# Kernel tuning notes

Hardware: AMD Instinct MI355X
Metric: run time of the kernel (lower is better)

The kernel has to match this reference:

```python
import jax, jax.numpy as jnp
import numpy as np

C = 64
SHIFT = 3
NEIGHBOR_SIZES = (3, 5, 7)  # dilation = 1 for all levels
NUM_GROUPS = 8


def conv2d(x, w, b, padding=0, groups=1):
    out = jax.lax.conv_general_dilated(
        x, w, (1, 1), [(padding, padding), (padding, padding)],
        dimension_numbers=('NCHW', 'OIHW', 'NCHW'),
        feature_group_count=groups)
    return out + b[None, :, None, None]


def natten_level(q, k, v, rpb, ks):
    # q,k,v: (B,H,W,C) channels-last; rpb: (2ks-1, 2ks-1); dilation=1.
    # NATTEN semantics: window of size ks x ks centered at each query, clamped
    # (shifted) at image borders so it always lies fully inside the image.
    B, H, W, Cc = q.shape
    r = ks // 2
    i = jnp.arange(H); ni = jnp.clip(i - r, 0, H - ks)   # window row starts
    j = jnp.arange(W); nj = jnp.clip(j - r, 0, W - ks)   # window col starts
    ar = jnp.arange(ks)
    ii = ni[:, None] + ar[None, :]                        # (H,ks) neighbor rows
    jj = nj[:, None] + ar[None, :]                        # (W,ks) neighbor cols
    kn = k[:, ii][:, :, :, jj]                            # (B,H,ks,W,ks,C)
    attn = jnp.einsum('bhwc,bhpwqc->bhwpq', q, kn)        # (B,H,W,ks,ks)
    # relative-position-bias lookup: row start pi = (ks-1) + ni - i
    pi = (ks - 1) + ni - i                                # (H,)
    pj = (ks - 1) + nj - j                                # (W,)
    bias = rpb[(pi[:, None] + ar[None, :])[:, None, :, None],
               (pj[:, None] + ar[None, :])[None, :, None, :]]  # (H,W,ks,ks)
    attn = attn + bias[None]
    attn = jax.nn.softmax(attn.reshape(B, H, W, ks * ks), axis=-1)
    attn = attn.reshape(B, H, W, ks, ks)
    vn = v[:, ii][:, :, :, jj]                            # (B,H,ks,W,ks,C)
    return jnp.einsum('bhwpq,bhpwqc->bhwc', attn, vn)


def _forward(sup_frame, key_frame, conv_smooth_w, conv_smooth_b,
             conv_reduce_w, conv_reduce_b, v_w0, v_b0, v_w1, v_b1,
             v_w2, v_b2, rpb0, rpb1, rpb2, fusion_w, fusion_b):
    p = SHIFT
    outs = [sup_frame]  # original (pre-shift) support features
    # shift-roll spatial correlation
    shifts = [(sh, sw) for sh in (-p, 0, p) for sw in (-p, 0, p)
              if not (sh == 0 and sw == 0)]
    padded = jnp.pad(sup_frame, ((0, 0), (0, 0), (p, p), (p, p)))
    parts = jnp.split(padded, NUM_GROUPS, axis=1)
    shifted = jnp.concatenate(
        [jnp.roll(parts[g], shifts[g], axis=(2, 3)) for g in range(NUM_GROUPS)],
        axis=1)[..., p:-p, p:-p]
    shifted = conv2d(shifted, conv_smooth_w, conv_smooth_b, padding=1,
                     groups=NUM_GROUPS)
    sup2 = conv2d(jnp.concatenate([sup_frame, shifted], axis=1),
                  conv_reduce_w, conv_reduce_b)
    # multi-scale neighborhood attention (single head)
    q = jnp.transpose(key_frame, (0, 2, 3, 1))
    k = jnp.transpose(sup2, (0, 2, 3, 1))
    v_ws = (v_w0, v_w1, v_w2); v_bs = (v_b0, v_b1, v_b2)
    rpbs = (rpb0, rpb1, rpb2)
    for lvl, ks in enumerate(NEIGHBOR_SIZES):
        v = jnp.transpose(conv2d(sup2, v_ws[lvl], v_bs[lvl]), (0, 2, 3, 1))
        agg = natten_level(q, k, v, rpbs[lvl], ks)
        outs.append(jnp.transpose(agg, (0, 3, 1, 2)))
    fused = jnp.concatenate(outs, axis=1)  # (B, 4*C, H, W)
    return jax.nn.relu(conv2d(fused, fusion_w, fusion_b, padding=1))


def setup_inputs() -> dict:
    key = jax.random.key(0)
    ks = jax.random.split(key, 20)
    B, H, W = 4, 96, 96
    s = 0.05
    d = {}
    d['sup_frame'] = jax.random.normal(ks[0], (B, C, H, W), jnp.float32)
    d['key_frame'] = jax.random.normal(ks[1], (B, C, H, W), jnp.float32)
    d['conv_smooth_w'] = jax.random.normal(ks[2], (C, C // NUM_GROUPS, 3, 3), jnp.float32) * s
    d['conv_smooth_b'] = jnp.zeros((C,), jnp.float32)
    d['conv_reduce_w'] = jax.random.normal(ks[3], (C, 2 * C, 1, 1), jnp.float32) * s
    d['conv_reduce_b'] = jnp.zeros((C,), jnp.float32)
    for i, nk in enumerate(NEIGHBOR_SIZES):
        d[f'v_w{i}'] = jax.random.normal(ks[4 + i], (C, C, 1, 1), jnp.float32) * s
        d[f'v_b{i}'] = jnp.zeros((C,), jnp.float32)
        d[f'rpb{i}'] = jax.random.normal(ks[8 + i], (2 * nk - 1, 2 * nk - 1), jnp.float32) * 0.02
    d['fusion_w'] = jax.random.normal(ks[12], (C, C * (len(NEIGHBOR_SIZES) + 1), 3, 3), jnp.float32) * s
    d['fusion_b'] = jnp.zeros((C,), jnp.float32)
    return d


def reference(sup_frame, key_frame, conv_smooth_w, conv_smooth_b,
              conv_reduce_w, conv_reduce_b, v_w0, v_b0, v_w1, v_b1,
              v_w2, v_b2, rpb0, rpb1, rpb2, fusion_w, fusion_b):
    return _forward(sup_frame, key_frame, conv_smooth_w, conv_smooth_b,
                    conv_reduce_w, conv_reduce_b, v_w0, v_b0, v_w1, v_b1,
                    v_w2, v_b2, rpb0, rpb1, rpb2, fusion_w, fusion_b)
```

## Files before the change

kernel.cpp:

```cpp
#include <hip/hip_runtime.h>
#include <hip/hip_bf16.h>

#define HW 9216
#define NPX 36864

typedef __attribute__((ext_vector_type(8))) short short8;
typedef __attribute__((ext_vector_type(4))) float f32x4;

static __device__ __forceinline__ unsigned short f2bf(float x) {
    union { __hip_bfloat16 h; unsigned short u; } c; c.h = __float2bfloat16(x); return c.u;
}
static __device__ __forceinline__ float bfl(unsigned int u){ return __uint_as_float(u << 16); }
static __device__ __forceinline__ float bfh(unsigned int u){ return __uint_as_float(u & 0xffff0000u); }

__global__ __launch_bounds__(256) void prep_weights(
    const float* __restrict__ rw, const float* __restrict__ vw0,
    const float* __restrict__ vw1, const float* __restrict__ vw2,
    const float* __restrict__ fw,
    float* __restrict__ rwT, unsigned short* __restrict__ vwF, unsigned short* __restrict__ fwF)
{
    int idx = blockIdx.x * 256 + threadIdx.x;
    if (idx < 8192) {
        int c = idx & 63, i = idx >> 6;
        rwT[idx] = rw[c * 128 + i];
    } else if (idx < 20480) {
        int e = idx - 8192;
        int j = e & 7, lane = (e >> 3) & 63, kf = (e >> 9) & 1, nt = (e >> 10) & 3, lvl = e >> 12;
        int co = nt * 16 + (lane & 15);
        int k = kf * 32 + (lane >> 4) * 8 + j;
        const float* vw = (lvl == 0) ? vw0 : ((lvl == 1) ? vw1 : vw2);
        vwF[e] = f2bf(vw[co * 64 + k]);
    } else if (idx < 167936) {
        int e = idx - 20480;
        int j = e & 7, lane = (e >> 3) & 63, nt = (e >> 9) & 3, kc = e >> 11;
        int co = nt * 16 + (lane & 15);
        int k = kc * 32 + ((lane >> 4) << 3) + j;
        int tap = k >> 8, ci = k & 255;
        fwF[e] = f2bf(fw[co * 2304 + ci * 9 + tap]);
    }
}

__global__ void pack_kernel(const float* __restrict__ key, const float* __restrict__ sup,
                            float* __restrict__ qT, __hip_bfloat16* __restrict__ fused)
{
    __shared__ float lk[32][33], ls[32][33];
    int tx = threadIdx.x, ty = threadIdx.y;
    int x0 = blockIdx.x * 32, c0 = blockIdx.y * 32;
    int z = blockIdx.z; int b = z / 96, y = z - b * 96;
    #pragma unroll
    for (int i = 0; i < 32; i += 8) {
        int c = c0 + ty + i;
        lk[ty + i][tx] = key[((b * 64 + c) * 96 + y) * 96 + x0 + tx];
        ls[ty + i][tx] = sup[((b * 64 + c) * 96 + y) * 96 + x0 + tx];
    }
    __syncthreads();
    #pragma unroll
    for (int i = 0; i < 32; i += 8) {
        int px = (b * 96 + y) * 96 + x0 + ty + i;
        qT[px * 64 + c0 + tx]     = lk[tx][ty + i];
        fused[px * 256 + c0 + tx] = __hip_bfloat16(ls[tx][ty + i]);
    }
}

__global__ __launch_bounds__(256) void shift_smooth(const float* __restrict__ sup,
    const float* __restrict__ w, const float* __restrict__ bias, float* __restrict__ smooth)
{
    __shared__ __align__(16) float tile[8][34][36];
    int bid = blockIdx.x;
    int half = bid & 1;
    int sj   = (bid >> 1) % 9;
    int grp  = (bid / 18) & 7;
    int b    = bid / 144;
    int sby = sj / 3, sbx = sj % 3;
    int Y0 = sby * 32, X0 = sbx * 32;
    int sh = 3 * ((grp >= 5) - (grp < 3));
    int mm = (grp < 3) ? grp : ((grp < 5) ? ((grp == 3) ? 0 : 2) : (grp - 5));
    int sw = 3 * mm - 3;
    int t = threadIdx.x;

    const float* supg = sup + (size_t)(b * 64 + grp * 8) * HW;
    #pragma unroll
    for (int pp = 0; pp < 5; pp++) {
        int pos = pp * 256 + t;
        if (pos < 1156) {
            int r = pos / 34, u = pos - r * 34;
            int yy = Y0 - 1 + r, xx = X0 - 1 + u;
            int ys = yy - sh, xs = xx - sw;
            bool ok = (yy >= 0) & (yy < 96) & (xx >= 0) & (xx < 96) &
                      (ys >= 0) & (ys < 96) & (xs >= 0) & (xs < 96);
            int addr = ok ? (ys * 96 + xs) : 0;
            #pragma unroll
            for (int ic = 0; ic < 8; ic++) {
                float v = supg[(size_t)ic * HW + addr];
                tile[ic][r][u] = ok ? v : 0.f;
            }
        }
    }
    __syncthreads();

    int c = __builtin_amdgcn_readfirstlane(grp * 8 + half * 4 + (t >> 6));
    int lane = t & 63;
    int ty4 = lane >> 3, tx4 = lane & 7;
    int py0 = ty4 * 4, x0r = tx4 * 4;

    float bz = bias[c];
    float acc[4][4];
    #pragma unroll
    for (int jr = 0; jr < 4; jr++)
        #pragma unroll
        for (int j = 0; j < 4; j++) acc[jr][j] = bz;

    const float* wp = w + c * 72;
    for (int ic = 0; ic < 8; ic++) {
        float wr[9];
        #pragma unroll
        for (int q = 0; q < 9; q++) wr[q] = wp[ic * 9 + q];
        #pragma unroll
        for (int rr = 0; rr < 6; rr++) {
            float4 fa = *(const float4*)&tile[ic][py0 + rr][x0r];
            float4 fb4 = *(const float4*)&tile[ic][py0 + rr][x0r + 4];
            float f[6] = {fa.x, fa.y, fa.z, fa.w, fb4.x, fb4.y};
            #pragma unroll
            for (int ky = 0; ky < 3; ky++) {
                int jr = rr - ky;
                if (jr >= 0 && jr < 4) {
                    #pragma unroll
                    for (int j = 0; j < 4; j++)
                        acc[jr][j] += wr[ky*3]*f[j] + wr[ky*3+1]*f[j+1] + wr[ky*3+2]*f[j+2];
                }
            }
        }
    }

    float* op = smooth + ((size_t)(b * 64 + c) * 96 + Y0 + py0) * 96 + X0 + x0r;
    #pragma unroll
    for (int jr = 0; jr < 4; jr++) {
        float4 st = {acc[jr][0], acc[jr][1], acc[jr][2], acc[jr][3]};
        *(float4*)(op + (size_t)jr * 96) = st;
    }
}

__global__ __launch_bounds__(256) void reduce_kernel(const float* __restrict__ sup,
    const float* __restrict__ smooth, const float* __restrict__ rwT,
    const float* __restrict__ rb, float* __restrict__ sup2)
{
    __shared__ __align__(16) float wlds[8192];
    int t = threadIdx.x;
    #pragma unroll
    for (int e = 0; e < 8; e++) {
        int idx = (e * 256 + t) * 4;
        *(float4*)&wlds[idx] = *(const float4*)&rwT[idx];
    }
    __syncthreads();

    int lane = t & 63, wq = t >> 6;
    int px = blockIdx.x * 64 + lane;
    int b = px / HW; int rem = px - b * HW;
    const float* s1 = sup + (size_t)b * 64 * HW + rem;
    const float* s2 = smooth + (size_t)b * 64 * HW + rem;
    float acc[16];
    #pragma unroll
    for (int j = 0; j < 16; j++) acc[j] = rb[wq * 16 + j];

    #pragma unroll 8
    for (int i = 0; i < 64; i++) {
        float v = s1[i * HW];
        const float* wr = &wlds[i * 64 + wq * 16];
        float4 w0 = *(const float4*)wr, w1 = *(const float4*)(wr + 4);
        float4 w2 = *(const float4*)(wr + 8), w3 = *(const float4*)(wr + 12);
        acc[0] += w0.x * v;  acc[1] += w0.y * v;  acc[2] += w0.z * v;  acc[3] += w0.w * v;
        acc[4] += w1.x * v;  acc[5] += w1.y * v;  acc[6] += w1.z * v;  acc[7] += w1.w * v;
        acc[8] += w2.x * v;  acc[9] += w2.y * v;  acc[10] += w2.z * v; acc[11] += w2.w * v;
        acc[12] += w3.x * v; acc[13] += w3.y * v; acc[14] += w3.z * v; acc[15] += w3.w * v;
    }
    #pragma unroll 8
    for (int i = 0; i < 64; i++) {
        float v = s2[i * HW];
        const float* wr = &wlds[(64 + i) * 64 + wq * 16];
        float4 w0 = *(const float4*)wr, w1 = *(const float4*)(wr + 4);
        float4 w2 = *(const float4*)(wr + 8), w3 = *(const float4*)(wr + 12);
        acc[0] += w0.x * v;  acc[1] += w0.y * v;  acc[2] += w0.z * v;  acc[3] += w0.w * v;
        acc[4] += w1.x * v;  acc[5] += w1.y * v;  acc[6] += w1.z * v;  acc[7] += w1.w * v;
        acc[8] += w2.x * v;  acc[9] += w2.y * v;  acc[10] += w2.z * v; acc[11] += w2.w * v;
        acc[12] += w3.x * v; acc[13] += w3.y * v; acc[14] += w3.z * v; acc[15] += w3.w * v;
    }

    float* op = sup2 + (size_t)px * 64 + wq * 16;
    #pragma unroll
    for (int j = 0; j < 16; j += 4) { float4 st = {acc[j], acc[j+1], acc[j+2], acc[j+3]}; *(float4*)(op + j) = st; }
}

template<int KS>
__device__ __forceinline__ void level_softmax(int qc, int y, int x, int ni7, int nj7,
        const _Float16* rpbl, const _Float16* dots_row, _Float16* out_row)
{
    constexpr int R = KS / 2, KK = KS * KS, NB = 2 * KS - 1;
    constexpr int NE = (KK + 3) / 4;
    int ni = min(max(y - R, 0), 96 - KS), nj = min(max(x - R, 0), 96 - KS);
    int di = ni - ni7, dj = nj - nj7;
    int br = KS - 1 + ni - y, bc = KS - 1 + nj - x;
    float sv[NE];
    float mx = -1e30f;
    #pragma unroll
    for (int i = 0; i < NE; i++) {
        int e = qc + i * 4;
        if (e < KK) {
            int ey = e / KS, ex = e - ey * KS;
            float s = (float)dots_row[(di + ey) * 7 + dj + ex] + (float)rpbl[(br + ey) * NB + bc + ex];
            sv[i] = s; mx = fmaxf(mx, s);
        } else sv[i] = -1e30f;
    }
    mx = fmaxf(mx, __shfl_xor(mx, 16)); mx = fmaxf(mx, __shfl_xor(mx, 32));
    float sum = 0.f;
    #pragma unroll
    for (int i = 0; i < NE; i++) { sv[i] = __expf(sv[i] - mx); sum += sv[i]; }
    sum += __shfl_xor(sum, 16); sum += __shfl_xor(sum, 32);
    float inv = 1.f / sum;
    #pragma unroll
    for (int i = 0; i < NE; i++) {
        int e = qc + i * 4;
        if (e < KK) out_row[e] = (_Float16)(sv[i] * inv);
    }
}

__global__ __launch_bounds__(256) void natten_fused(
    const float* __restrict__ qT, const float* __restrict__ sup2,
    const unsigned short* __restrict__ vwF,
    const float* __restrict__ vb0, const float* __restrict__ vb1, const float* __restrict__ vb2,
    const float* __restrict__ rpb0, const float* __restrict__ rpb1, const float* __restrict__ rpb2,
    __hip_bfloat16* __restrict__ fused)
{
    __shared__ __align__(16) unsigned short khalo[196 * 72];
    __shared__ _Float16 dots[64][52];
    __shared__ _Float16 a3[64][12];
    __shared__ _Float16 a5[64][28];
    __shared__ _Float16 rlds[276];

    int t = threadIdx.x;
    int bb = blockIdx.y;
    int tx0 = (blockIdx.x % 12) * 8, ty0 = (blockIdx.x / 12) * 8;
    const float* kb = sup2 + (size_t)bb * HW * 64;

    for (int e = t; e < 275; e += 256) {
        float v = (e < 169) ? rpb2[e] : ((e < 250) ? rpb1[e - 169] : rpb0[e - 250]);
        rlds[e] = (_Float16)v;
    }

    for (int it = 0; it < 13; it++) {
        int qidx = it * 256 + t;
        if (qidx < 3136) {
            int cq = qidx & 15, pos = qidx >> 4;
            int py = pos / 14, pxx = pos - py * 14;
            int gy = min(max(ty0 - 3 + py, 0), 95);
            int gx = min(max(tx0 - 3 + pxx, 0), 95);
            float4 v = *(const float4*)(kb + (((size_t)gy * 96 + gx) << 6) + cq * 4);
            ushort4 pk = {f2bf(v.x), f2bf(v.y), f2bf(v.z), f2bf(v.w)};
            *(ushort4*)&khalo[pos * 72 + cq * 4] = pk;
        }
    }
    __syncthreads();

    int lane = t & 63, wv = t >> 6;
    int pxl = wv * 16 + (lane & 15);
    int qc = lane >> 4;
    int pty = pxl >> 3, ptx = pxl & 7;
    int y = ty0 + pty, x = tx0 + ptx;
    int gpx = bb * HW + y * 96 + x;

    float qv[16];
    {
        const float* qp = qT + (size_t)gpx * 64 + qc * 16;
        #pragma unroll
        for (int j = 0; j < 16; j += 4) {
            float4 q4 = *(const float4*)(qp + j);
            qv[j] = q4.x; qv[j+1] = q4.y; qv[j+2] = q4.z; qv[j+3] = q4.w;
        }
    }

    int ni7 = min(max(y - 3, 0), 89), nj7 = min(max(x - 3, 0), 89);
    int ly = ni7 - (ty0 - 3), lx = nj7 - (tx0 - 3);

    for (int oy = 0; oy < 7; oy++) {
        #pragma unroll
        for (int ox = 0; ox < 7; ox++) {
            const unsigned short* kp = &khalo[((ly + oy) * 14 + lx + ox) * 72 + qc * 16];
            uint4 ka = *(const uint4*)kp;
            uint4 kc = *(const uint4*)(kp + 8);
            float p0 = qv[0]*bfl(ka.x) + qv[1]*bfh(ka.x) + qv[2]*bfl(ka.y) + qv[3]*bfh(ka.y);
            float p1 = qv[4]*bfl(ka.z) + qv[5]*bfh(ka.z) + qv[6]*bfl(ka.w) + qv[7]*bfh(ka.w);
            float p2 = qv[8]*bfl(kc.x) + qv[9]*bfh(kc.x) + qv[10]*bfl(kc.y) + qv[11]*bfh(kc.y);
            float p3 = qv[12]*bfl(kc.z) + qv[13]*bfh(kc.z) + qv[14]*bfl(kc.w) + qv[15]*bfh(kc.w);
            float d = (p0 + p1) + (p2 + p3);
            d += __shfl_xor(d, 16);
            d += __shfl_xor(d, 32);
            if (qc == 0) dots[pxl][oy * 7 + ox] = (_Float16)d;
        }
    }

    level_softmax<3>(qc, y, x, ni7, nj7, rlds + 250, &dots[pxl][0], &a3[pxl][0]);
    level_softmax<5>(qc, y, x, ni7, nj7, rlds + 169, &dots[pxl][0], &a5[pxl][0]);
    level_softmax<7>(qc, y, x, ni7, nj7, rlds,       &dots[pxl][0], &dots[pxl][0]);

    int ni5 = min(max(y - 2, 0), 91), nj5 = min(max(x - 2, 0), 91);
    int ni3 = min(max(y - 1, 0), 93), nj3 = min(max(x - 1, 0), 93);
    int di5 = ni5 - ni7, dj5 = nj5 - nj7, di3 = ni3 - ni7, dj3 = nj3 - nj7;

    float s2[3][16];
    #pragma unroll
    for (int l = 0; l < 3; l++)
        #pragma unroll
        for (int j = 0; j < 16; j++) s2[l][j] = 0.f;

    for (int oy = 0; oy < 7; oy++) {
        #pragma unroll
        for (int ox = 0; ox < 7; ox++) {
            const unsigned short* kp = &khalo[((ly + oy) * 14 + lx + ox) * 72 + qc * 16];
            uint4 ka = *(const uint4*)kp;
            uint4 kc = *(const uint4*)(kp + 8);
            float kv[16] = {bfl(ka.x), bfh(ka.x), bfl(ka.y), bfh(ka.y),
                            bfl(ka.z), bfh(ka.z), bfl(ka.w), bfh(ka.w),
                            bfl(kc.x), bfh(kc.x), bfl(kc.y), bfh(kc.y),
                            bfl(kc.z), bfh(kc.z), bfl(kc.w), bfh(kc.w)};
            float w7 = (float)dots[pxl][oy * 7 + ox];
            #pragma unroll
            for (int j = 0; j < 16; j++) s2[2][j] += w7 * kv[j];
            int e5y = oy - di5, e5x = ox - dj5;
            if ((unsigned)e5y < 5u && (unsigned)e5x < 5u) {
                float w5 = (float)a5[pxl][e5y * 5 + e5x];
                #pragma unroll
                for (int j = 0; j < 16; j++) s2[1][j] += w5 * kv[j];
            }
            int e3y = oy - di3, e3x = ox - dj3;
            if ((unsigned)e3y < 3u && (unsigned)e3x < 3u) {
                float w3 = (float)a3[pxl][e3y * 3 + e3x];
                #pragma unroll
                for (int j = 0; j < 16; j++) s2[0][j] += w3 * kv[j];
            }
        }
    }
    __syncthreads();

    unsigned short* sproj = khalo;
    #pragma unroll
    for (int l = 0; l < 3; l++) {
        unsigned int pk[8];
        #pragma unroll
        for (int j = 0; j < 8; j++)
            pk[j] = (unsigned int)f2bf(s2[l][2*j]) | ((unsigned int)f2bf(s2[l][2*j+1]) << 16);
        unsigned int* dst = (unsigned int*)&sproj[(l * 64 + pxl) * 72 + qc * 16];
        uint4 s0 = {pk[0], pk[1], pk[2], pk[3]};
        uint4 s1 = {pk[4], pk[5], pk[6], pk[7]};
        *(uint4*)dst = s0;
        *(uint4*)(dst + 4) = s1;
    }
    __syncthreads();

    int lm = lane & 15, quad = lane >> 4;
    #pragma unroll
    for (int l = 0; l < 3; l++) {
        f32x4 acc[4];
        #pragma unroll
        for (int nt = 0; nt < 4; nt++) acc[nt] = (f32x4){0.f, 0.f, 0.f, 0.f};
        #pragma unroll
        for (int kf = 0; kf < 2; kf++) {
            short8 a = *(const short8*)&sproj[(l * 64 + wv * 16 + lm) * 72 + kf * 32 + quad * 8];
            #pragma unroll
            for (int nt = 0; nt < 4; nt++) {
                short8 bfr = *(const short8*)&vwF[(((l * 4 + nt) * 2 + kf) * 64 + lane) * 8];
                acc[nt] = __builtin_amdgcn_mfma_f32_16x16x32_bf16(a, bfr, acc[nt], 0, 0, 0);
            }
        }
        const float* vbl = (l == 0) ? vb0 : ((l == 1) ? vb1 : vb2);
        #pragma unroll
        for (int nt = 0; nt < 4; nt++)
            #pragma unroll
            for (int r = 0; r < 4; r++) {
                int p = wv * 16 + quad * 4 + r;
                int co = nt * 16 + lm;
                int py = p >> 3, pxx = p & 7;
                size_t off = ((size_t)(bb * HW + (ty0 + py) * 96 + tx0 + pxx) << 8) + (l + 1) * 64 + co;
                fused[off] = __hip_bfloat16(acc[nt][r] + vbl[co]);
            }
    }
}

__global__ __launch_bounds__(256) void fusion_mfma(
    const __hip_bfloat16* __restrict__ fB, const unsigned short* __restrict__ fwF,
    const float* __restrict__ fb, float* __restrict__ out)
{
    __shared__ __align__(16) unsigned short ah[108 * 72];
    __shared__ float lds_out[64 * 66];
    int t = threadIdx.x;
    int wv = t >> 6, lane = t & 63, lm = lane & 15, quad = lane >> 4;
    int X0 = blockIdx.x * 16, Y0 = blockIdx.y * 4, b = blockIdx.z;
    const unsigned short* fBu = (const unsigned short*)fB;

    f32x4 acc[4] = {};

    for (int chunk = 0; chunk < 4; chunk++) {
        __syncthreads();
        #pragma unroll
        for (int ee = 0; ee < 4; ee++) {
            int e = ee * 256 + t;
            if (e < 864) {
                int seg = e & 7, hp = e >> 3;
                int hy = hp / 18, hx = hp - hy * 18;
                int gy = Y0 - 1 + hy, gx = X0 - 1 + hx;
                bool ok = (gy >= 0) & (gy < 96) & (gx >= 0) & (gx < 96);
                short8 v = {};
                if (ok) v = *(const short8*)(fBu + (((size_t)(b * HW + gy * 96 + gx)) << 8) + chunk * 64 + seg * 8);
                *(short8*)&ah[hp * 72 + seg * 8] = v;
            }
        }
        __syncthreads();
        #pragma unroll
        for (int ky = 0; ky < 3; ky++) {
            #pragma unroll
            for (int kx = 0; kx < 3; kx++) {
                #pragma unroll
                for (int kf = 0; kf < 2; kf++) {
                    short8 a = *(const short8*)&ah[((wv + ky) * 18 + lm + kx) * 72 + kf * 32 + quad * 8];
                    int kc = (ky * 3 + kx) * 8 + chunk * 2 + kf;
                    const unsigned short* bp = fwF + ((size_t)(kc * 4) * 64 + lane) * 8;
                    acc[0] = __builtin_amdgcn_mfma_f32_16x16x32_bf16(a, *(const short8*)(bp),        acc[0], 0, 0, 0);
                    acc[1] = __builtin_amdgcn_mfma_f32_16x16x32_bf16(a, *(const short8*)(bp + 512),  acc[1], 0, 0, 0);
                    acc[2] = __builtin_amdgcn_mfma_f32_16x16x32_bf16(a, *(const short8*)(bp + 1024), acc[2], 0, 0, 0);
                    acc[3] = __builtin_amdgcn_mfma_f32_16x16x32_bf16(a, *(const short8*)(bp + 1536), acc[3], 0, 0, 0);
                }
            }
        }
    }

    #pragma unroll
    for (int nt = 0; nt < 4; nt++)
        #pragma unroll
        for (int r = 0; r < 4; r++) {
            int p = wv * 16 + quad * 4 + r;
            int co = nt * 16 + lm;
            lds_out[co * 66 + p] = acc[nt][r];
        }
    __syncthreads();

    int p2 = t & 63, py = p2 >> 4, px2 = p2 & 15;
    float* ob = out + ((size_t)(b * 64) * 96 + Y0 + py) * 96 + X0 + px2;
    #pragma unroll 4
    for (int i = 0; i < 16; i++) {
        int co = (t >> 6) * 16 + i;
        float v = lds_out[co * 66 + p2] + fb[co];
        ob[(size_t)co * HW] = v > 0.f ? v : 0.f;
    }
}

extern "C" void kernel_launch(void* const* d_in, const int* in_sizes, int n_in,
                              void* d_out, int out_size, void* d_ws, size_t ws_size,
                              hipStream_t stream) {
    const float* sup = (const float*)d_in[0];
    const float* key = (const float*)d_in[1];
    const float* smw = (const float*)d_in[2];
    const float* smb = (const float*)d_in[3];
    const float* rw  = (const float*)d_in[4];
    const float* rb  = (const float*)d_in[5];
    const float *vw[3], *vb[3], *rpb[3];
    if (in_sizes[8] == 25) {
        for (int l = 0; l < 3; l++) {
            vw[l]  = (const float*)d_in[6 + 3 * l];
            vb[l]  = (const float*)d_in[7 + 3 * l];
            rpb[l] = (const float*)d_in[8 + 3 * l];
        }
    } else {
        for (int l = 0; l < 3; l++) {
            vw[l]  = (const float*)d_in[6 + 2 * l];
            vb[l]  = (const float*)d_in[7 + 2 * l];
            rpb[l] = (const float*)d_in[12 + l];
        }
    }
    const float* fw = (const float*)d_in[15];
    const float* fb = (const float*)d_in[16];
    float* out = (float*)d_out;

    float* wsf    = (float*)d_ws;
    float* smooth = wsf;
    float* sup2   = wsf + 2359296;
    float* qT     = wsf + 4718592;
    float* rwT    = wsf + 7077888;
    unsigned short* vwF = (unsigned short*)(wsf + 7086080);
    __hip_bfloat16* fusedB = (__hip_bfloat16*)(wsf + 7092224);
    unsigned short* fwF    = (unsigned short*)(wsf + 11810816);

    prep_weights<<<dim3(656), dim3(256), 0, stream>>>(rw, vw[0], vw[1], vw[2], fw, rwT, vwF, fwF);
    pack_kernel<<<dim3(3, 2, 384), dim3(32, 8), 0, stream>>>(key, sup, qT, fusedB);
    shift_smooth<<<dim3(576), dim3(256), 0, stream>>>(sup, smw, smb, smooth);
    reduce_kernel<<<dim3(576), dim3(256), 0, stream>>>(sup, smooth, rwT, rb, sup2);
    natten_fused<<<dim3(144, 4), dim3(256), 0, stream>>>(qT, sup2, vwF,
        vb[0], vb[1], vb[2], rpb[0], rpb[1], rpb[2], fusedB);
    fusion_mfma<<<dim3(6, 24, 4), dim3(256), 0, stream>>>(fusedB, fwF, fb, out);
}
```

Baseline: 225.3 us.

## Halve natten tile to 8x4 pixels with 8 lanes per pixel for more blocks

The natten kernel now processes an 8x4 pixel tile per block instead of 8x8, with 8 threads per pixel each handling 8 channels rather than 4 threads handling 16. The grid doubles to 288x4 blocks, shared memory per block shrinks, and per-thread register use for accumulators drops, aiming at higher occupancy and better spread across CUs. In exchange the halo load grows relative to useful work, dot and softmax reductions need an extra shuffle stage, and only 3 of 4 waves run the MFMA projection.

New measurement: 278.2 us. +23.5%, slower.

```diff
diff --git a/kernel.cpp b/kernel.cpp
--- a/kernel.cpp
+++ b/kernel.cpp
@@ -195,7 +195,7 @@
         const _Float16* rpbl, const _Float16* dots_row, _Float16* out_row)
 {
     constexpr int R = KS / 2, KK = KS * KS, NB = 2 * KS - 1;
-    constexpr int NE = (KK + 3) / 4;
+    constexpr int NE = (KK + 7) / 8;
     int ni = min(max(y - R, 0), 96 - KS), nj = min(max(x - R, 0), 96 - KS);
     int di = ni - ni7, dj = nj - nj7;
     int br = KS - 1 + ni - y, bc = KS - 1 + nj - x;
@@ -203,22 +203,22 @@
     float mx = -1e30f;
     #pragma unroll
     for (int i = 0; i < NE; i++) {
-        int e = qc + i * 4;
+        int e = qc + i * 8;
         if (e < KK) {
             int ey = e / KS, ex = e - ey * KS;
             float s = (float)dots_row[(di + ey) * 7 + dj + ex] + (float)rpbl[(br + ey) * NB + bc + ex];
             sv[i] = s; mx = fmaxf(mx, s);
         } else sv[i] = -1e30f;
     }
-    mx = fmaxf(mx, __shfl_xor(mx, 16)); mx = fmaxf(mx, __shfl_xor(mx, 32));
+    mx = fmaxf(mx, __shfl_xor(mx, 8)); mx = fmaxf(mx, __shfl_xor(mx, 16)); mx = fmaxf(mx, __shfl_xor(mx, 32));
     float sum = 0.f;
     #pragma unroll
     for (int i = 0; i < NE; i++) { sv[i] = __expf(sv[i] - mx); sum += sv[i]; }
-    sum += __shfl_xor(sum, 16); sum += __shfl_xor(sum, 32);
+    sum += __shfl_xor(sum, 8); sum += __shfl_xor(sum, 16); sum += __shfl_xor(sum, 32);
     float inv = 1.f / sum;
     #pragma unroll
     for (int i = 0; i < NE; i++) {
-        int e = qc + i * 4;
+        int e = qc + i * 8;
         if (e < KK) out_row[e] = (_Float16)(sv[i] * inv);
     }
 }
@@ -230,15 +230,15 @@
     const float* __restrict__ rpb0, const float* __restrict__ rpb1, const float* __restrict__ rpb2,
     __hip_bfloat16* __restrict__ fused)
 {
-    __shared__ __align__(16) unsigned short khalo[196 * 72];
-    __shared__ _Float16 dots[64][52];
-    __shared__ _Float16 a3[64][12];
-    __shared__ _Float16 a5[64][28];
+    __shared__ __align__(16) unsigned short khalo[140 * 72];
+    __shared__ _Float16 dots[32][52];
+    __shared__ _Float16 a3[32][12];
+    __shared__ _Float16 a5[32][28];
     __shared__ _Float16 rlds[276];
 
     int t = threadIdx.x;
     int bb = blockIdx.y;
-    int tx0 = (blockIdx.x % 12) * 8, ty0 = (blockIdx.x / 12) * 8;
+    int tx0 = (blockIdx.x % 12) * 8, ty0 = (blockIdx.x / 12) * 4;
     const float* kb = sup2 + (size_t)bb * HW * 64;
 
     for (int e = t; e < 275; e += 256) {
@@ -246,9 +246,9 @@
         rlds[e] = (_Float16)v;
     }
 
-    for (int it = 0; it < 13; it++) {
+    for (int it = 0; it < 9; it++) {
         int qidx = it * 256 + t;
-        if (qidx < 3136) {
+        if (qidx < 2240) {
             int cq = qidx & 15, pos = qidx >> 4;
             int py = pos / 14, pxx = pos - py * 14;
             int gy = min(max(ty0 - 3 + py, 0), 95);
@@ -261,20 +261,18 @@
     __syncthreads();
 
     int lane = t & 63, wv = t >> 6;
-    int pxl = wv * 16 + (lane & 15);
-    int qc = lane >> 4;
+    int pxl = wv * 8 + (lane & 7);
+    int qc = lane >> 3;
     int pty = pxl >> 3, ptx = pxl & 7;
     int y = ty0 + pty, x = tx0 + ptx;
     int gpx = bb * HW + y * 96 + x;
 
-    float qv[16];
+    float qv[8];
     {
-        const float* qp = qT + (size_t)gpx * 64 + qc * 16;
-        #pragma unroll
-        for (int j = 0; j < 16; j += 4) {
-            float4 q4 = *(const float4*)(qp + j);
-            qv[j] = q4.x; qv[j+1] = q4.y; qv[j+2] = q4.z; qv[j+3] = q4.w;
-        }
+        const float* qp = qT + (size_t)gpx * 64 + qc * 8;
+        float4 q0 = *(const float4*)qp, q1 = *(const float4*)(qp + 4);
+        qv[0] = q0.x; qv[1] = q0.y; qv[2] = q0.z; qv[3] = q0.w;
+        qv[4] = q1.x; qv[5] = q1.y; qv[6] = q1.z; qv[7] = q1.w;
     }
 
     int ni7 = min(max(y - 3, 0), 89), nj7 = min(max(x - 3, 0), 89);
@@ -283,14 +281,12 @@
     for (int oy = 0; oy < 7; oy++) {
         #pragma unroll
         for (int ox = 0; ox < 7; ox++) {
-            const unsigned short* kp = &khalo[((ly + oy) * 14 + lx + ox) * 72 + qc * 16];
+            const unsigned short* kp = &khalo[((ly + oy) * 14 + lx + ox) * 72 + qc * 8];
             uint4 ka = *(const uint4*)kp;
-            uint4 kc = *(const uint4*)(kp + 8);
             float p0 = qv[0]*bfl(ka.x) + qv[1]*bfh(ka.x) + qv[2]*bfl(ka.y) + qv[3]*bfh(ka.y);
             float p1 = qv[4]*bfl(ka.z) + qv[5]*bfh(ka.z) + qv[6]*bfl(ka.w) + qv[7]*bfh(ka.w);
-            float p2 = qv[8]*bfl(kc.x) + qv[9]*bfh(kc.x) + qv[10]*bfl(kc.y) + qv[11]*bfh(kc.y);
-            float p3 = qv[12]*bfl(kc.z) + qv[13]*bfh(kc.z) + qv[14]*bfl(kc.w) + qv[15]*bfh(kc.w);
-            float d = (p0 + p1) + (p2 + p3);
+            float d = p0 + p1;
+            d += __shfl_xor(d, 8);
             d += __shfl_xor(d, 16);
             d += __shfl_xor(d, 32);
             if (qc == 0) dots[pxl][oy * 7 + ox] = (_Float16)d;
@@ -305,36 +301,33 @@
     int ni3 = min(max(y - 1, 0), 93), nj3 = min(max(x - 1, 0), 93);
     int di5 = ni5 - ni7, dj5 = nj5 - nj7, di3 = ni3 - ni7, dj3 = nj3 - nj7;
 
-    float s2[3][16];
+    float s2[3][8];
     #pragma unroll
     for (int l = 0; l < 3; l++)
         #pragma unroll
-        for (int j = 0; j < 16; j++) s2[l][j] = 0.f;
+        for (int j = 0; j < 8; j++) s2[l][j] = 0.f;
 
     for (int oy = 0; oy < 7; oy++) {
         #pragma unroll
         for (int ox = 0; ox < 7; ox++) {
-            const unsigned short* kp = &khalo[((ly + oy) * 14 + lx + ox) * 72 + qc * 16];
+            const unsigned short* kp = &khalo[((ly + oy) * 14 + lx + ox) * 72 + qc * 8];
             uint4 ka = *(const uint4*)kp;
-            uint4 kc = *(const uint4*)(kp + 8);
-            float kv[16] = {bfl(ka.x), bfh(ka.x), bfl(ka.y), bfh(ka.y),
-                            bfl(ka.z), bfh(ka.z), bfl(ka.w), bfh(ka.w),
-                            bfl(kc.x), bfh(kc.x), bfl(kc.y), bfh(kc.y),
-                            bfl(kc.z), bfh(kc.z), bfl(kc.w), bfh(kc.w)};
+            float kv[8] = {bfl(ka.x), bfh(ka.x), bfl(ka.y), bfh(ka.y),
+                           bfl(ka.z), bfh(ka.z), bfl(ka.w), bfh(ka.w)};
             float w7 = (float)dots[pxl][oy * 7 + ox];
             #pragma unroll
-            for (int j = 0; j < 16; j++) s2[2][j] += w7 * kv[j];
+            for (int j = 0; j < 8; j++) s2[2][j] += w7 * kv[j];
             int e5y = oy - di5, e5x = ox - dj5;
             if ((unsigned)e5y < 5u && (unsigned)e5x < 5u) {
                 float w5 = (float)a5[pxl][e5y * 5 + e5x];
                 #pragma unroll
-                for (int j = 0; j < 16; j++) s2[1][j] += w5 * kv[j];
+                for (int j = 0; j < 8; j++) s2[1][j] += w5 * kv[j];
             }
             int e3y = oy - di3, e3x = ox - dj3;
             if ((unsigned)e3y < 3u && (unsigned)e3x < 3u) {
                 float w3 = (float)a3[pxl][e3y * 3 + e3x];
                 #pragma unroll
-                for (int j = 0; j < 16; j++) s2[0][j] += w3 * kv[j];
+                for (int j = 0; j < 8; j++) s2[0][j] += w3 * kv[j];
             }
         }
     }
@@ -343,44 +336,44 @@
     unsigned short* sproj = khalo;
     #pragma unroll
     for (int l = 0; l < 3; l++) {
-        unsigned int pk[8];
-        #pragma unroll
-        for (int j = 0; j < 8; j++)
+        unsigned int pk[4];
+        #pragma unroll
+        for (int j = 0; j < 4; j++)
             pk[j] = (unsigned int)f2bf(s2[l][2*j]) | ((unsigned int)f2bf(s2[l][2*j+1]) << 16);
-        unsigned int* dst = (unsigned int*)&sproj[(l * 64 + pxl) * 72 + qc * 16];
-        uint4 s0 = {pk[0], pk[1], pk[2], pk[3]};
-        uint4 s1 = {pk[4], pk[5], pk[6], pk[7]};
-        *(uint4*)dst = s0;
-        *(uint4*)(dst + 4) = s1;
-    }
-    __syncthreads();
-
-    int lm = lane & 15, quad = lane >> 4;
-    #pragma unroll
-    for (int l = 0; l < 3; l++) {
-        f32x4 acc[4];
-        #pragma unroll
-        for (int nt = 0; nt < 4; nt++) acc[nt] = (f32x4){0.f, 0.f, 0.f, 0.f};
-        #pragma unroll
-        for (int kf = 0; kf < 2; kf++) {
-            short8 a = *(const short8*)&sproj[(l * 64 + wv * 16 + lm) * 72 + kf * 32 + quad * 8];
-            #pragma unroll
-            for (int nt = 0; nt < 4; nt++) {
-                short8 bfr = *(const short8*)&vwF[(((l * 4 + nt) * 2 + kf) * 64 + lane) * 8];
-                acc[nt] = __builtin_amdgcn_mfma_f32_16x16x32_bf16(a, bfr, acc[nt], 0, 0, 0);
-            }
-        }
+        uint4 sv = {pk[0], pk[1], pk[2], pk[3]};
+        *(uint4*)&sproj[(l * 32 + pxl) * 72 + qc * 8] = sv;
+    }
+    __syncthreads();
+
+    if (wv < 3) {
+        int l = wv;
+        int lm = lane & 15, quad = lane >> 4;
         const float* vbl = (l == 0) ? vb0 : ((l == 1) ? vb1 : vb2);
         #pragma unroll
-        for (int nt = 0; nt < 4; nt++)
-            #pragma unroll
-            for (int r = 0; r < 4; r++) {
-                int p = wv * 16 + quad * 4 + r;
-                int co = nt * 16 + lm;
-                int py = p >> 3, pxx = p & 7;
-                size_t off = ((size_t)(bb * HW + (ty0 + py) * 96 + tx0 + pxx) << 8) + (l + 1) * 64 + co;
-                fused[off] = __hip_bfloat16(acc[nt][r] + vbl[co]);
-            }
+        for (int mt = 0; mt < 2; mt++) {
+            f32x4 acc[4];
+            #pragma unroll
+            for (int nt = 0; nt < 4; nt++) acc[nt] = (f32x4){0.f, 0.f, 0.f, 0.f};
+            #pragma unroll
+            for (int kf = 0; kf < 2; kf++) {
+                short8 a = *(const short8*)&sproj[(l * 32 + mt * 16 + lm) * 72 + kf * 32 + quad * 8];
+                #pragma unroll
+                for (int nt = 0; nt < 4; nt++) {
+                    short8 bfr = *(const short8*)&vwF[(((l * 4 + nt) * 2 + kf) * 64 + lane) * 8];
+                    acc[nt] = __builtin_amdgcn_mfma_f32_16x16x32_bf16(a, bfr, acc[nt], 0, 0, 0);
+                }
+            }
+            #pragma unroll
+            for (int nt = 0; nt < 4; nt++)
+                #pragma unroll
+                for (int r = 0; r < 4; r++) {
+                    int p = mt * 16 + quad * 4 + r;
+                    int co = nt * 16 + lm;
+                    int py = p >> 3, pxx = p & 7;
+                    size_t off = ((size_t)(bb * HW + (ty0 + py) * 96 + tx0 + pxx) << 8) + (l + 1) * 64 + co;
+                    fused[off] = __hip_bfloat16(acc[nt][r] + vbl[co]);
+                }
+        }
     }
 }
 
@@ -491,7 +484,7 @@
     pack_kernel<<<dim3(3, 2, 384), dim3(32, 8), 0, stream>>>(key, sup, qT, fusedB);
     shift_smooth<<<dim3(576), dim3(256), 0, stream>>>(sup, smw, smb, smooth);
     reduce_kernel<<<dim3(576), dim3(256), 0, stream>>>(sup, smooth, rwT, rb, sup2);
-    natten_fused<<<dim3(144, 4), dim3(256), 0, stream>>>(qT, sup2, vwF,
+    natten_fused<<<dim3(288, 4), dim3(256), 0, stream>>>(qT, sup2, vwF,
         vb[0], vb[1], vb[2], rpb[0], rpb[1], rpb[2], fusedB);
     fusion_mfma<<<dim3(6, 24, 4), dim3(256), 0, stream>>>(fusedB, fwF, fb, out);
 }
```
